# Optimization experiments

Measured on AMD Instinct MI355X. Metric: run time of the kernel, lower is better.

The kernel has to match this reference:

```python
import jax, jax.numpy as jnp
import numpy as np

EPS = 1e-12

def _l2norm(x):
    # F.normalize(x, p=2, dim=1) applied on [B*N, D] == normalize last dim of [B, N, D]
    return x / jnp.maximum(jnp.linalg.norm(x, axis=-1, keepdims=True), EPS)

def setup_inputs() -> dict:
    key = jax.random.key(0)
    k1, k2 = jax.random.split(key)
    B, N, D = 128, 64, 128  # batch_size, num_epoch, feature_dim
    feat_k = jax.random.normal(k1, (B, N, D), dtype=jnp.float32)
    feat_q = jax.random.normal(k2, (B, N, D), dtype=jnp.float32)
    return {"feat_k": feat_k, "feat_q": feat_q}

def reference(feat_k, feat_q):
    B, N, D = feat_k.shape
    fk = _l2norm(feat_k)                       # [B, N, D]
    fq = jax.lax.stop_gradient(_l2norm(feat_q))  # sampler branch is no_grad

    # Dense pairwise similarities, as in the original einsum('ijk,mnk->ijnm')
    logits = jnp.einsum('ijk,mnk->ijnm', fk, fk)  # [B, N, N, B]
    sim    = jnp.einsum('ijk,mnk->ijnm', fq, fq)  # [B, N, N, B]

    el = jnp.exp(logits)

    # mask[i, j, n, m] = (m == i):
    #   pos[i, j] = sum_n exp(logits[i, j, n, i])
    pos = jnp.einsum('ijni->ij', el)              # diagonal over (i, m), summed over n

    #   neg[i, j] = sum_{n, m != i} exp(logits[i, j, n, m]) * sim[i, j, n, m]
    prod = el * sim
    neg = prod.sum(axis=(2, 3)) - jnp.einsum('ijni->ij', prod)

    loss = jnp.mean(-jnp.log(pos / (pos + neg)))
    return loss
```

## Files before the change

kernel.cpp:

```cpp
#include <hip/hip_runtime.h>
#include <stdint.h>

#define ROWS 8192
#define D    128
#define CSPLIT 16
#define CPS  (ROWS / CSPLIT)
#define BM   256
#define BN   64
#define NT   (CPS / BN)
#define SQRT_LOG2E 1.2011224087864498f

typedef __bf16 bf16x8 __attribute__((ext_vector_type(8)));
typedef float  f32x4  __attribute__((ext_vector_type(4)));

typedef const __attribute__((address_space(1))) uint32_t guint;
typedef __attribute__((address_space(3))) uint32_t luint;

__device__ __forceinline__ void gload_lds16(const void* g, void* l) {
    __builtin_amdgcn_global_load_lds((guint*)g, (luint*)l, 16, 0, 0);
}

__device__ __forceinline__ ushort f2bf(float f) {
    union { float f; uint32_t u; } x; x.f = f;
    uint32_t r = x.u + 0x7FFFu + ((x.u >> 16) & 1u);
    return (ushort)(r >> 16);
}

__global__ __launch_bounds__(256) void k_norm(
    const float* __restrict__ fk, const float* __restrict__ fq,
    ushort* __restrict__ fkn, ushort* __restrict__ fqn)
{
    int gw = (blockIdx.x * 256 + threadIdx.x) >> 6;
    int l  = threadIdx.x & 63;
    const float* src; ushort* dst; int r; float scale;
    if (gw < ROWS) { src = fk; dst = fkn; r = gw; scale = SQRT_LOG2E; }
    else           { src = fq; dst = fqn; r = gw - ROWS; scale = 1.0f; }
    float2 v = *reinterpret_cast<const float2*>(&src[r * D + l * 2]);
    float ss = v.x * v.x + v.y * v.y;
    #pragma unroll
    for (int m = 1; m < 64; m <<= 1) ss += __shfl_xor(ss, m, 64);
    float inv = scale / fmaxf(sqrtf(ss), 1e-12f);
    ushort2 o; o.x = f2bf(v.x * inv); o.y = f2bf(v.y * inv);
    *reinterpret_cast<ushort2*>(&dst[r * D + l * 2]) = o;
}

__global__ __launch_bounds__(256, 2) void k_gram(
    const ushort* __restrict__ fkn, const ushort* __restrict__ fqn,
    float* __restrict__ pneg, float* __restrict__ ppos)
{
    __shared__ ushort lds[2][2 * BN * D];
    const int rt = blockIdx.x;
    const int cs = blockIdx.y;
    const int w  = threadIdx.x >> 6;
    const int l  = threadIdx.x & 63;
    const int lrow = l >> 4, lcol = l & 15;
    const int r0 = rt * BM;

    int off[4];
    #pragma unroll
    for (int t = 0; t < 4; ++t) {
        int L = t * 256 + w * 64 + l;
        int row = L >> 4, slot = L & 15;
        int col = slot ^ (row & 7);
        off[t] = row * 256 + col * 16;
    }

    auto issue_stage = [&](int buf, int cbase) {
        const char* fkb = (const char*)fkn + (size_t)cbase * 256;
        const char* fqb = (const char*)fqn + (size_t)cbase * 256;
        #pragma unroll
        for (int t = 0; t < 4; ++t) {
            gload_lds16(fkb + off[t], &lds[buf][t * 2048 + w * 512]);
            gload_lds16(fqb + off[t], &lds[buf][BN * D + t * 2048 + w * 512]);
        }
    };

    issue_stage(0, cs * CPS);

    bf16x8 ak[4][4], aq[4][4];
    #pragma unroll
    for (int rg = 0; rg < 4; ++rg) {
        int arow = r0 + w * 64 + rg * 16 + lcol;
        #pragma unroll
        for (int ks = 0; ks < 4; ++ks) {
            ak[rg][ks] = *reinterpret_cast<const bf16x8*>(fkn + arow * D + ks * 32 + lrow * 8);
            aq[rg][ks] = *reinterpret_cast<const bf16x8*>(fqn + arow * D + ks * 32 + lrow * 8);
        }
    }

    const int diagc = r0 + w * 64;

    float accp[4][4] = {};
    float accn[4][4] = {};

    __syncthreads();

    int cur = 0;
    for (int t = 0; t < NT; ++t) {
        const int cbase = cs * CPS + t * BN;
        if (t + 1 < NT) issue_stage(cur ^ 1, cbase + BN);
        const bool diag = (cbase == diagc);
        const ushort* bkb = &lds[cur][0];
        const ushort* bqb = &lds[cur][BN * D];
        #pragma unroll
        for (int cc = 0; cc < 4; ++cc) {
            int brow = cc * 16 + lcol;
            f32x4 sk[4] = {{0,0,0,0},{0,0,0,0},{0,0,0,0},{0,0,0,0}};
            f32x4 sq[4] = {{0,0,0,0},{0,0,0,0},{0,0,0,0},{0,0,0,0}};
            #pragma unroll
            for (int ks = 0; ks < 4; ++ks) {
                int slot = (ks * 4 + lrow) ^ (brow & 7);
                bf16x8 bk = *reinterpret_cast<const bf16x8*>(bkb + brow * D + slot * 8);
                bf16x8 bq = *reinterpret_cast<const bf16x8*>(bqb + brow * D + slot * 8);
                #pragma unroll
                for (int rg = 0; rg < 4; ++rg) {
                    sk[rg] = __builtin_amdgcn_mfma_f32_16x16x32_bf16(ak[rg][ks], bk, sk[rg], 0, 0, 0);
                    sq[rg] = __builtin_amdgcn_mfma_f32_16x16x32_bf16(aq[rg][ks], bq, sq[rg], 0, 0, 0);
                }
            }
            if (diag) {
                #pragma unroll
                for (int rg = 0; rg < 4; ++rg)
                    #pragma unroll
                    for (int e = 0; e < 4; ++e)
                        accp[rg][e] += __builtin_exp2f(sk[rg][e]);
            } else {
                #pragma unroll
                for (int rg = 0; rg < 4; ++rg)
                    #pragma unroll
                    for (int e = 0; e < 4; ++e)
                        accn[rg][e] += __builtin_exp2f(sk[rg][e]) * sq[rg][e];
            }
        }
        __syncthreads();
        cur ^= 1;
    }

    #pragma unroll
    for (int m = 1; m <= 8; m <<= 1) {
        #pragma unroll
        for (int rg = 0; rg < 4; ++rg)
            #pragma unroll
            for (int e = 0; e < 4; ++e) {
                accp[rg][e] += __shfl_xor(accp[rg][e], m, 64);
                accn[rg][e] += __shfl_xor(accn[rg][e], m, 64);
            }
    }
    if (lcol == 0) {
        #pragma unroll
        for (int rg = 0; rg < 4; ++rg)
            #pragma unroll
            for (int e = 0; e < 4; ++e) {
                int gr = r0 + w * 64 + rg * 16 + lrow * 4 + e;
                ppos[cs * ROWS + gr] = accp[rg][e];
                pneg[cs * ROWS + gr] = accn[rg][e];
            }
    }
}

__global__ __launch_bounds__(256) void k_loss1(
    const float* __restrict__ pneg, const float* __restrict__ ppos,
    float* __restrict__ bsum)
{
    int r = blockIdx.x * 256 + threadIdx.x;
    float pos = 0.f, neg = 0.f;
    #pragma unroll
    for (int p = 0; p < CSPLIT; ++p) { pos += ppos[p * ROWS + r]; neg += pneg[p * ROWS + r]; }
    float s = log1pf(neg / pos);
    #pragma unroll
    for (int m = 1; m < 64; m <<= 1) s += __shfl_xor(s, m, 64);
    __shared__ float red[4];
    if ((threadIdx.x & 63) == 0) red[threadIdx.x >> 6] = s;
    __syncthreads();
    if (threadIdx.x == 0) bsum[blockIdx.x] = red[0] + red[1] + red[2] + red[3];
}

__global__ void k_loss2(const float* __restrict__ bsum, float* __restrict__ out)
{
    int l = threadIdx.x;
    float s = (l < 32) ? bsum[l] : 0.f;
    #pragma unroll
    for (int m = 1; m < 64; m <<= 1) s += __shfl_xor(s, m, 64);
    if (l == 0) out[0] = s * (1.0f / ROWS);
}

extern "C" void kernel_launch(void* const* d_in, const int* in_sizes, int n_in,
                              void* d_out, int out_size, void* d_ws, size_t ws_size,
                              hipStream_t stream)
{
    const float* fk = (const float*)d_in[0];
    const float* fq = (const float*)d_in[1];
    ushort* fkn = (ushort*)d_ws;
    ushort* fqn = fkn + ROWS * D;
    float*  pneg = (float*)(fqn + ROWS * D);
    float*  ppos = pneg + CSPLIT * ROWS;
    float*  bsum = ppos + CSPLIT * ROWS;

    k_norm<<<(2 * ROWS) / 4, 256, 0, stream>>>(fk, fq, fkn, fqn);
    k_gram<<<dim3(ROWS / BM, CSPLIT), 256, 0, stream>>>(fkn, fqn, pneg, ppos);
    k_loss1<<<32, 256, 0, stream>>>(pneg, ppos, bsum);
    k_loss2<<<1, 64, 0, stream>>>(bsum, (float*)d_out);
}
```

Baseline: 55.90 us.

## Enlarge gram blocks to 512 threads, square tiles, and specialize diagonal tile path

Each gram block now covers 512 rows with 8 waves and shares each staged 64-column LDS tile across twice as many A rows, halving B-tile global traffic per row. The grid becomes a square 16x16 grid, so the diagonal tile is known statically and its wave skips the fq MFMAs and writes pos directly. This removes the partial pos buffers and their reduction. B fragments are preloaded before the MFMA chain, with s_setprio raised around the MFMAs. The cost is more threads per block, which may lower occupancy and raise register pressure.

```diff
diff --git a/kernel.cpp b/kernel.cpp
--- a/kernel.cpp
+++ b/kernel.cpp
@@ -4,10 +4,10 @@
 #define ROWS 8192
 #define D    128
 #define CSPLIT 16
-#define CPS  (ROWS / CSPLIT)
-#define BM   256
+#define CPS  512
+#define BM   512
 #define BN   64
-#define NT   (CPS / BN)
+#define NT   8
 #define SQRT_LOG2E 1.2011224087864498f
 
 typedef __bf16 bf16x8 __attribute__((ext_vector_type(8)));
@@ -44,7 +44,7 @@
     *reinterpret_cast<ushort2*>(&dst[r * D + l * 2]) = o;
 }
 
-__global__ __launch_bounds__(256, 2) void k_gram(
+__global__ __launch_bounds__(512, 2) void k_gram(
     const ushort* __restrict__ fkn, const ushort* __restrict__ fqn,
     float* __restrict__ pneg, float* __restrict__ ppos)
 {
@@ -55,27 +55,28 @@
     const int l  = threadIdx.x & 63;
     const int lrow = l >> 4, lcol = l & 15;
     const int r0 = rt * BM;
-
-    int off[4];
-    #pragma unroll
-    for (int t = 0; t < 4; ++t) {
-        int L = t * 256 + w * 64 + l;
+    const int cbase0 = cs * CPS;
+
+    int off[2];
+    #pragma unroll
+    for (int i = 0; i < 2; ++i) {
+        int L = w * 128 + i * 64 + l;
         int row = L >> 4, slot = L & 15;
-        int col = slot ^ (row & 7);
-        off[t] = row * 256 + col * 16;
+        off[i] = row * 256 + (slot ^ (row & 7)) * 16;
     }
 
     auto issue_stage = [&](int buf, int cbase) {
         const char* fkb = (const char*)fkn + (size_t)cbase * 256;
         const char* fqb = (const char*)fqn + (size_t)cbase * 256;
-        #pragma unroll
-        for (int t = 0; t < 4; ++t) {
-            gload_lds16(fkb + off[t], &lds[buf][t * 2048 + w * 512]);
-            gload_lds16(fqb + off[t], &lds[buf][BN * D + t * 2048 + w * 512]);
-        }
+        ushort* lk = &lds[buf][w * 1024];
+        ushort* lq = &lds[buf][BN * D + w * 1024];
+        gload_lds16(fkb + off[0], lk);
+        gload_lds16(fkb + off[1], lk + 512);
+        gload_lds16(fqb + off[0], lq);
+        gload_lds16(fqb + off[1], lq + 512);
     };
 
-    issue_stage(0, cs * CPS);
+    issue_stage(0, cbase0);
 
     bf16x8 ak[4][4], aq[4][4];
     #pragma unroll
@@ -88,43 +89,75 @@
         }
     }
 
-    const int diagc = r0 + w * 64;
-
-    float accp[4][4] = {};
     float accn[4][4] = {};
 
     __syncthreads();
 
-    int cur = 0;
     for (int t = 0; t < NT; ++t) {
-        const int cbase = cs * CPS + t * BN;
-        if (t + 1 < NT) issue_stage(cur ^ 1, cbase + BN);
-        const bool diag = (cbase == diagc);
+        const int cur = t & 1;
+        if (t + 1 < NT) issue_stage(cur ^ 1, cbase0 + (t + 1) * BN);
         const ushort* bkb = &lds[cur][0];
         const ushort* bqb = &lds[cur][BN * D];
-        #pragma unroll
-        for (int cc = 0; cc < 4; ++cc) {
-            int brow = cc * 16 + lcol;
-            f32x4 sk[4] = {{0,0,0,0},{0,0,0,0},{0,0,0,0},{0,0,0,0}};
-            f32x4 sq[4] = {{0,0,0,0},{0,0,0,0},{0,0,0,0},{0,0,0,0}};
-            #pragma unroll
-            for (int ks = 0; ks < 4; ++ks) {
-                int slot = (ks * 4 + lrow) ^ (brow & 7);
-                bf16x8 bk = *reinterpret_cast<const bf16x8*>(bkb + brow * D + slot * 8);
-                bf16x8 bq = *reinterpret_cast<const bf16x8*>(bqb + brow * D + slot * 8);
-                #pragma unroll
-                for (int rg = 0; rg < 4; ++rg) {
-                    sk[rg] = __builtin_amdgcn_mfma_f32_16x16x32_bf16(ak[rg][ks], bk, sk[rg], 0, 0, 0);
-                    sq[rg] = __builtin_amdgcn_mfma_f32_16x16x32_bf16(aq[rg][ks], bq, sq[rg], 0, 0, 0);
+        const bool dtile = (cs == rt) && (t == w);
+        if (dtile) {
+            float posa[4][4] = {};
+            #pragma unroll
+            for (int cc = 0; cc < 4; ++cc) {
+                int brow = cc * 16 + lcol;
+                bf16x8 bk[4];
+                #pragma unroll
+                for (int ks = 0; ks < 4; ++ks) {
+                    int slot = (ks * 4 + lrow) ^ (brow & 7);
+                    bk[ks] = *reinterpret_cast<const bf16x8*>(bkb + brow * 128 + slot * 8);
                 }
-            }
-            if (diag) {
-                #pragma unroll
-                for (int rg = 0; rg < 4; ++rg)
-                    #pragma unroll
-                    for (int e = 0; e < 4; ++e)
-                        accp[rg][e] += __builtin_exp2f(sk[rg][e]);
-            } else {
+                f32x4 sk[4] = {{0,0,0,0},{0,0,0,0},{0,0,0,0},{0,0,0,0}};
+                #pragma unroll
+                for (int ks = 0; ks < 4; ++ks)
+                    #pragma unroll
+                    for (int rg = 0; rg < 4; ++rg)
+                        sk[rg] = __builtin_amdgcn_mfma_f32_16x16x32_bf16(ak[rg][ks], bk[ks], sk[rg], 0, 0, 0);
+                #pragma unroll
+                for (int rg = 0; rg < 4; ++rg)
+                    #pragma unroll
+                    for (int e = 0; e < 4; ++e)
+                        posa[rg][e] += __builtin_exp2f(sk[rg][e]);
+            }
+            #pragma unroll
+            for (int m = 1; m <= 8; m <<= 1)
+                #pragma unroll
+                for (int rg = 0; rg < 4; ++rg)
+                    #pragma unroll
+                    for (int e = 0; e < 4; ++e)
+                        posa[rg][e] += __shfl_xor(posa[rg][e], m, 64);
+            if (lcol == 0) {
+                #pragma unroll
+                for (int rg = 0; rg < 4; ++rg)
+                    #pragma unroll
+                    for (int e = 0; e < 4; ++e)
+                        ppos[r0 + w * 64 + rg * 16 + lrow * 4 + e] = posa[rg][e];
+            }
+        } else {
+            #pragma unroll
+            for (int cc = 0; cc < 4; ++cc) {
+                int brow = cc * 16 + lcol;
+                bf16x8 bk[4], bq[4];
+                #pragma unroll
+                for (int ks = 0; ks < 4; ++ks) {
+                    int slot = (ks * 4 + lrow) ^ (brow & 7);
+                    bk[ks] = *reinterpret_cast<const bf16x8*>(bkb + brow * 128 + slot * 8);
+                    bq[ks] = *reinterpret_cast<const bf16x8*>(bqb + brow * 128 + slot * 8);
+                }
+                f32x4 sk[4] = {{0,0,0,0},{0,0,0,0},{0,0,0,0},{0,0,0,0}};
+                f32x4 sq[4] = {{0,0,0,0},{0,0,0,0},{0,0,0,0},{0,0,0,0}};
+                __builtin_amdgcn_s_setprio(1);
+                #pragma unroll
+                for (int ks = 0; ks < 4; ++ks)
+                    #pragma unroll
+                    for (int rg = 0; rg < 4; ++rg) {
+                        sk[rg] = __builtin_amdgcn_mfma_f32_16x16x32_bf16(ak[rg][ks], bk[ks], sk[rg], 0, 0, 0);
+                        sq[rg] = __builtin_amdgcn_mfma_f32_16x16x32_bf16(aq[rg][ks], bq[ks], sq[rg], 0, 0, 0);
+                    }
+                __builtin_amdgcn_s_setprio(0);
                 #pragma unroll
                 for (int rg = 0; rg < 4; ++rg)
                     #pragma unroll
@@ -133,26 +166,21 @@
             }
         }
         __syncthreads();
-        cur ^= 1;
-    }
-
-    #pragma unroll
-    for (int m = 1; m <= 8; m <<= 1) {
+    }
+
+    #pragma unroll
+    for (int m = 1; m <= 8; m <<= 1)
         #pragma unroll
         for (int rg = 0; rg < 4; ++rg)
             #pragma unroll
-            for (int e = 0; e < 4; ++e) {
-                accp[rg][e] += __shfl_xor(accp[rg][e], m, 64);
+            for (int e = 0; e < 4; ++e)
                 accn[rg][e] += __shfl_xor(accn[rg][e], m, 64);
-            }
-    }
     if (lcol == 0) {
         #pragma unroll
         for (int rg = 0; rg < 4; ++rg)
             #pragma unroll
             for (int e = 0; e < 4; ++e) {
                 int gr = r0 + w * 64 + rg * 16 + lrow * 4 + e;
-                ppos[cs * ROWS + gr] = accp[rg][e];
                 pneg[cs * ROWS + gr] = accn[rg][e];
             }
     }
@@ -163,9 +191,10 @@
     float* __restrict__ bsum)
 {
     int r = blockIdx.x * 256 + threadIdx.x;
-    float pos = 0.f, neg = 0.f;
-    #pragma unroll
-    for (int p = 0; p < CSPLIT; ++p) { pos += ppos[p * ROWS + r]; neg += pneg[p * ROWS + r]; }
+    float pos = ppos[r];
+    float neg = 0.f;
+    #pragma unroll
+    for (int p = 0; p < CSPLIT; ++p) neg += pneg[p * ROWS + r];
     float s = log1pf(neg / pos);
     #pragma unroll
     for (int m = 1; m < 64; m <<= 1) s += __shfl_xor(s, m, 64);
@@ -194,10 +223,10 @@
     ushort* fqn = fkn + ROWS * D;
     float*  pneg = (float*)(fqn + ROWS * D);
     float*  ppos = pneg + CSPLIT * ROWS;
-    float*  bsum = ppos + CSPLIT * ROWS;
+    float*  bsum = ppos + ROWS;
 
     k_norm<<<(2 * ROWS) / 4, 256, 0, stream>>>(fk, fq, fkn, fqn);
-    k_gram<<<dim3(ROWS / BM, CSPLIT), 256, 0, stream>>>(fkn, fqn, pneg, ppos);
+    k_gram<<<dim3(16, 16), 512, 0, stream>>>(fkn, fqn, pneg, ppos);
     k_loss1<<<32, 256, 0, stream>>>(pneg, ppos, bsum);
     k_loss2<<<1, 64, 0, stream>>>(bsum, (float*)d_out);
 }
```

Measured after the change: 141.4 us. 2.53x slower.
